# Performance work log

Measured on AMD Instinct MI355X. Metric: run time of the kernel, lower is better.

## Reference

```python
import jax, jax.numpy as jnp
import numpy as np

N_NODES = 50000
N_EDGES = 800000
DIM_IN = 128
DIM_OUT = 64


def setup_inputs() -> dict:
    key = jax.random.key(0)
    k1, k2, k3, k4 = jax.random.split(key, 4)
    x = jax.random.normal(k1, (N_NODES, DIM_IN), dtype=jnp.float32)
    edge_index = jax.random.randint(k2, (2, N_EDGES), 0, N_NODES, dtype=jnp.int64)
    W = jax.random.normal(k3, (DIM_IN, DIM_OUT), dtype=jnp.float32) / np.sqrt(DIM_IN)
    b = jax.random.normal(k4, (DIM_OUT,), dtype=jnp.float32) * 0.01
    return {"x": x, "edge_index": edge_index, "W": W, "b": b}


def reference(x, edge_index, W, b):
    # Faithful PyG GCNConv: add self-loops, symmetric deg normalization,
    # linear transform then normalized scatter-add aggregation, then bias.
    N = x.shape[0]
    h = x @ W  # [N, dim_out] — transform before propagate (PyG order)

    loops = jnp.arange(N, dtype=edge_index.dtype)
    src = jnp.concatenate([edge_index[0], loops])  # [E+N]
    dst = jnp.concatenate([edge_index[1], loops])  # [E+N]

    ones = jnp.ones(src.shape[0], dtype=h.dtype)
    deg = jax.ops.segment_sum(ones, dst, num_segments=N)  # in-degree incl. self-loop
    dinv = jnp.where(deg > 0, jax.lax.rsqrt(deg), 0.0)
    norm = dinv[src] * dinv[dst]  # [E+N]

    msgs = h[src] * norm[:, None]  # gather + scale
    out = jax.ops.segment_sum(msgs, dst, num_segments=N) + b  # scatter-add
    return jax.nn.log_softmax(out, axis=1)
```

## Files before the change

### kernel.cpp

```cpp
#include <hip/hip_runtime.h>
#include <hip/hip_fp16.h>
#include <cstdint>
#include <cstddef>

#define N_NODES 50000
#define N_EDGES 800000
#define DIM_IN  128
#define DIM_OUT 64

#define B2SHIFT 8
#define B2NODES 256
#define NB2     ((N_NODES + B2NODES - 1) / B2NODES)
#define EB      4096
#define SORTB   ((N_EDGES + EB - 1) / EB)
#define NE4     (N_EDGES / 4)
#define CAPB    4864
#define GROWS   512
#define GEMMB   ((N_NODES + GROWS - 1) / GROWS)
#define GPAD    16
#define NEGRP   ((N_NODES + 31) / 32)

typedef _Float16 f16x8 __attribute__((ext_vector_type(8)));
typedef float    f32x4 __attribute__((ext_vector_type(4)));

__global__ __launch_bounds__(256) void k_zero(int* __restrict__ gcnt) {
    const int i = blockIdx.x * 256 + threadIdx.x;
    if (i < NB2 * GPAD) gcnt[i] = 0;
}

__global__ __launch_bounds__(1024) void kFG(const int* __restrict__ ei,
                                            int* __restrict__ gcnt,
                                            unsigned* __restrict__ pairs,
                                            const float* __restrict__ x,
                                            const float* __restrict__ W,
                                            __half* __restrict__ h) {
    const int t = threadIdx.x;
    if (blockIdx.x < SORTB) {
        __shared__ int hcnt[B2NODES];
        __shared__ int excl[B2NODES];
        __shared__ int curb[B2NODES];
        __shared__ int gbase[B2NODES];
        __shared__ int wsum[4];
        __shared__ unsigned lpair[EB];
        const int blk = blockIdx.x;
        const int ecnt = min(EB, N_EDGES - blk * EB);
        if (t < B2NODES) hcnt[t] = 0;
        __syncthreads();
        const int4* src4 = (const int4*)ei;
        const int4* dst4 = (const int4*)(ei + N_EDGES);
        const int g = blk * (EB / 4) + t;
        int4 sv, dv;
        const bool live = (g < NE4);
        if (live) {
            dv = dst4[g];
            sv = src4[g];
            atomicAdd(&hcnt[dv.x >> B2SHIFT], 1);
            atomicAdd(&hcnt[dv.y >> B2SHIFT], 1);
            atomicAdd(&hcnt[dv.z >> B2SHIFT], 1);
            atomicAdd(&hcnt[dv.w >> B2SHIFT], 1);
        }
        __syncthreads();
        if (t < B2NODES) {
            const int lane = t & 63;
            const int v = hcnt[t];
            int xs = v;
#pragma unroll
            for (int off = 1; off < 64; off <<= 1) {
                int y = __shfl_up(xs, off);
                if (lane >= off) xs += y;
            }
            excl[t] = xs;
            if (lane == 63) wsum[t >> 6] = xs;
        }
        __syncthreads();
        if (t == 0) {
            int acc = 0;
#pragma unroll
            for (int w2 = 0; w2 < 4; ++w2) { const int v2 = wsum[w2]; wsum[w2] = acc; acc += v2; }
        }
        __syncthreads();
        if (t < B2NODES) {
            const int v = hcnt[t];
            const int e = excl[t] - v + wsum[t >> 6];
            excl[t] = e;
            curb[t] = e;
            const int base = v ? atomicAdd(&gcnt[t * GPAD], v) : 0;
            gbase[t] = t * CAPB + base - e;
        }
        __syncthreads();
        if (live) {
            int b, p;
            b = dv.x >> B2SHIFT; p = atomicAdd(&curb[b], 1);
            lpair[p] = ((unsigned)sv.x << 16) | (unsigned)dv.x;
            b = dv.y >> B2SHIFT; p = atomicAdd(&curb[b], 1);
            lpair[p] = ((unsigned)sv.y << 16) | (unsigned)dv.y;
            b = dv.z >> B2SHIFT; p = atomicAdd(&curb[b], 1);
            lpair[p] = ((unsigned)sv.z << 16) | (unsigned)dv.z;
            b = dv.w >> B2SHIFT; p = atomicAdd(&curb[b], 1);
            lpair[p] = ((unsigned)sv.w << 16) | (unsigned)dv.w;
        }
        __syncthreads();
        for (int j = t; j < ecnt; j += 1024) {
            const unsigned p = lpair[j];
            const int b = (int)(p & 0xFFFFu) >> B2SHIFT;
            const int dst = gbase[b] + j;
            if (dst < (b + 1) * CAPB) pairs[dst] = p;
        }
    } else {
        const int u = blockIdx.x - SORTB;
        const int w = t >> 6;
        const int l = t & 63;
        const int q = l >> 4;
        const int m16 = l & 15;

        f16x8 bf[4][4];
#pragma unroll
        for (int kc = 0; kc < 4; ++kc)
#pragma unroll
            for (int ct = 0; ct < 4; ++ct) {
                const float* wp = W + (size_t)(kc * 32 + q * 8) * DIM_OUT + ct * 16 + m16;
                f16x8 v;
#pragma unroll
                for (int j = 0; j < 8; ++j) v[j] = (_Float16)wp[(size_t)j * DIM_OUT];
                bf[kc][ct] = v;
            }

        const int base = u * GROWS + w * 32;
#pragma unroll
        for (int rt = 0; rt < 2; ++rt) {
            const int m0 = base + rt * 16;
            int mrow = m0 + m16;
            if (mrow >= N_NODES) mrow = N_NODES - 1;

            f16x8 af[4];
#pragma unroll
            for (int kc = 0; kc < 4; ++kc) {
                const float4* xp = (const float4*)(x + (size_t)mrow * DIM_IN + kc * 32 + q * 8);
                const float4 p0 = xp[0], p1 = xp[1];
                f16x8 a;
                a[0] = (_Float16)p0.x; a[1] = (_Float16)p0.y;
                a[2] = (_Float16)p0.z; a[3] = (_Float16)p0.w;
                a[4] = (_Float16)p1.x; a[5] = (_Float16)p1.y;
                a[6] = (_Float16)p1.z; a[7] = (_Float16)p1.w;
                af[kc] = a;
            }

            f32x4 acc[4];
#pragma unroll
            for (int ct = 0; ct < 4; ++ct) acc[ct] = (f32x4){0.f, 0.f, 0.f, 0.f};
#pragma unroll
            for (int kc = 0; kc < 4; ++kc)
#pragma unroll
                for (int ct = 0; ct < 4; ++ct)
                    acc[ct] = __builtin_amdgcn_mfma_f32_16x16x32_f16(af[kc], bf[kc][ct], acc[ct], 0, 0, 0);

#pragma unroll
            for (int reg = 0; reg < 4; ++reg) {
                const int r = m0 + q * 4 + reg;
                if (r < N_NODES) {
#pragma unroll
                    for (int ct = 0; ct < 4; ++ct)
                        h[(size_t)r * DIM_OUT + ct * 16 + m16] = __float2half(acc[ct][reg]);
                }
            }
        }
    }
}

__global__ __launch_bounds__(512) void kSort(const unsigned* __restrict__ pairs,
                                             const int* __restrict__ gcnt,
                                             unsigned short* __restrict__ csr,
                                             int2* __restrict__ nodeoff2,
                                             __half* __restrict__ h) {
    __shared__ int cnt[B2NODES];
    __shared__ int cur[B2NODES];
    __shared__ float sdinv[B2NODES];
    __shared__ int wsum[4];
    __shared__ unsigned short lcsr[CAPB];
    const int b = blockIdx.x, t = threadIdx.x;
    const int eb = b * CAPB;
    const int count = min(gcnt[b * GPAD], CAPB);
    const int ee = eb + count;

    if (t < B2NODES) cnt[t] = 0;
    __syncthreads();

    {
        int i = eb + t;
        for (; i + 1536 < ee; i += 2048) {
            const unsigned p0 = pairs[i];
            const unsigned p1 = pairs[i + 512];
            const unsigned p2 = pairs[i + 1024];
            const unsigned p3 = pairs[i + 1536];
            atomicAdd(&cnt[p0 & (B2NODES - 1)], 1);
            atomicAdd(&cnt[p1 & (B2NODES - 1)], 1);
            atomicAdd(&cnt[p2 & (B2NODES - 1)], 1);
            atomicAdd(&cnt[p3 & (B2NODES - 1)], 1);
        }
        for (; i < ee; i += 512) atomicAdd(&cnt[pairs[i] & (B2NODES - 1)], 1);
    }
    __syncthreads();

    if (t < B2NODES) {
        const int lane = t & 63;
        const int v = cnt[t];
        int xs = v;
#pragma unroll
        for (int off = 1; off < 64; off <<= 1) {
            int y = __shfl_up(xs, off);
            if (lane >= off) xs += y;
        }
        cur[t] = xs;
        if (lane == 63) wsum[t >> 6] = xs;
    }
    __syncthreads();
    if (t == 0) {
        int acc = 0;
#pragma unroll
        for (int w2 = 0; w2 < 4; ++w2) { const int v2 = wsum[w2]; wsum[w2] = acc; acc += v2; }
    }
    __syncthreads();
    if (t < B2NODES) {
        const int v = cnt[t];
        const int excl = cur[t] - v + wsum[t >> 6];
        sdinv[t] = rsqrtf((float)(v + 1));
        const int n = (b << B2SHIFT) + t;
        if (n < N_NODES) nodeoff2[n] = make_int2(eb + excl, v);
        cur[t] = excl;
    }
    __syncthreads();

    for (int i = eb + t; i < ee; i += 512) {
        const unsigned p = pairs[i];
        const int q = atomicAdd(&cur[p & (B2NODES - 1)], 1);
        lcsr[q] = (unsigned short)(p >> 16);
    }
    __syncthreads();

    {
        const int cw = (count + 1) >> 1;
        const unsigned* l32 = (const unsigned*)lcsr;
        unsigned* c32 = (unsigned*)(csr + eb);
        for (int i2 = t; i2 < cw; i2 += 512) c32[i2] = l32[i2];
    }
    {
        f16x8* h8w = (f16x8*)h;
        for (int idx = t; idx < B2NODES * 8; idx += 512) {
            const int r = idx >> 3;
            const int n = (b << B2SHIFT) + r;
            if (n < N_NODES) {
                const float d = sdinv[r];
                f16x8 v = h8w[(size_t)n * 8 + (idx & 7)];
#pragma unroll
                for (int j = 0; j < 8; ++j) v[j] = (_Float16)((float)v[j] * d);
                h8w[(size_t)n * 8 + (idx & 7)] = v;
            }
        }
    }
}

__global__ __launch_bounds__(256) void kE_agg(const int2* __restrict__ nodeoff2,
                                              const unsigned short* __restrict__ csr,
                                              const __half* __restrict__ h,
                                              const float* __restrict__ bvec,
                                              float* __restrict__ out) {
    const int t = threadIdx.x;
    const int ew = t >> 3, sl = t & 7;
    const int n = blockIdx.x * 32 + ew;
    if (n >= N_NODES) return;
    const f16x8* __restrict__ h8 = (const f16x8*)h;

    const int2 off = nodeoff2[n];
    const int s0 = off.x, s1 = off.x + off.y;

    const f16x8 hv = h8[(size_t)n * 8 + sl];
    float a[8];
#pragma unroll
    for (int j = 0; j < 8; ++j) a[j] = (float)hv[j];

    int i = s0;
    for (; i + 4 <= s1; i += 4) {
        const int c0 = csr[i + 0];
        const int c1 = csr[i + 1];
        const int c2 = csr[i + 2];
        const int c3 = csr[i + 3];
        const f16x8 v0 = h8[(size_t)c0 * 8 + sl];
        const f16x8 v1 = h8[(size_t)c1 * 8 + sl];
        const f16x8 v2 = h8[(size_t)c2 * 8 + sl];
        const f16x8 v3 = h8[(size_t)c3 * 8 + sl];
#pragma unroll
        for (int j = 0; j < 8; ++j)
            a[j] += (float)v0[j] + (float)v1[j] + (float)v2[j] + (float)v3[j];
    }
    for (; i < s1; ++i) {
        const f16x8 v0 = h8[(size_t)csr[i] * 8 + sl];
#pragma unroll
        for (int j = 0; j < 8; ++j) a[j] += (float)v0[j];
    }

    const float4 b0 = *(const float4*)&bvec[8 * sl];
    const float4 b1 = *(const float4*)&bvec[8 * sl + 4];
    const float di = rsqrtf((float)(off.y + 1));
    float v[8];
    v[0] = a[0] * di + b0.x; v[1] = a[1] * di + b0.y;
    v[2] = a[2] * di + b0.z; v[3] = a[3] * di + b0.w;
    v[4] = a[4] * di + b1.x; v[5] = a[5] * di + b1.y;
    v[6] = a[6] * di + b1.z; v[7] = a[7] * di + b1.w;

    float m = v[0];
#pragma unroll
    for (int j = 1; j < 8; ++j) m = fmaxf(m, v[j]);
#pragma unroll
    for (int o = 4; o > 0; o >>= 1) m = fmaxf(m, __shfl_xor(m, o));
    float s = 0.f;
#pragma unroll
    for (int j = 0; j < 8; ++j) s += __expf(v[j] - m);
#pragma unroll
    for (int o = 4; o > 0; o >>= 1) s += __shfl_xor(s, o);
    const float ls = m + __logf(s);

    float4 o0, o1;
    o0.x = v[0] - ls; o0.y = v[1] - ls; o0.z = v[2] - ls; o0.w = v[3] - ls;
    o1.x = v[4] - ls; o1.y = v[5] - ls; o1.z = v[6] - ls; o1.w = v[7] - ls;
    *(float4*)&out[(size_t)n * DIM_OUT + 8 * sl]     = o0;
    *(float4*)&out[(size_t)n * DIM_OUT + 8 * sl + 4] = o1;
}

extern "C" void kernel_launch(void* const* d_in, const int* in_sizes, int n_in,
                              void* d_out, int out_size, void* d_ws, size_t ws_size,
                              hipStream_t stream) {
    const float* x  = (const float*)d_in[0];
    const int*   ei = (const int*)d_in[1];
    const float* W  = (const float*)d_in[2];
    const float* b  = (const float*)d_in[3];
    float* out = (float*)d_out;

    char* ws = (char*)d_ws;
    __half*         h        = (__half*)ws;         ws += (size_t)N_NODES * DIM_OUT * sizeof(__half);
    unsigned*       pairs    = (unsigned*)ws;       ws += (size_t)NB2 * CAPB * sizeof(unsigned);
    unsigned short* csr      = (unsigned short*)ws; ws += (size_t)NB2 * CAPB * sizeof(unsigned short);
    int2*           nodeoff2 = (int2*)ws;           ws += (size_t)N_NODES * sizeof(int2);
    int*            gcnt     = (int*)ws;            ws += (size_t)NB2 * GPAD * sizeof(int);

    k_zero <<<(NB2 * GPAD + 255) / 256, 256, 0, stream>>>(gcnt);
    kFG    <<<SORTB + GEMMB, 1024, 0, stream>>>(ei, gcnt, pairs, x, W, h);
    kSort  <<<NB2, 512, 0, stream>>>(pairs, gcnt, csr, nodeoff2, h);
    kE_agg <<<NEGRP, 256, 0, stream>>>(nodeoff2, csr, h, b, out);
}
```

Before: 122.3 us.

## Replace global atomic bucket counters with per-block histogram and deterministic prefix scatter

Splits the fused histogram+scatter stage into a histogram kernel (fused with the GEMM) that writes per-block bucket counts, and a separate scatter kernel that computes each block's global offsets by summing earlier blocks' histograms. This removes the zeroing kernel and global atomics on bucket counters, and makes pair placement deterministic. The cost is an extra kernel launch, the edge index being read twice, and an O(SORTB) serial prefix loop per bucket thread in kScatter. kSort now reduces the histogram column to get its bucket total. GEMM blocks shrink to 256 threads with 128 rows each.

```diff
diff --git a/kernel.cpp b/kernel.cpp
--- a/kernel.cpp
+++ b/kernel.cpp
@@ -15,80 +15,155 @@
 #define SORTB   ((N_EDGES + EB - 1) / EB)
 #define NE4     (N_EDGES / 4)
 #define CAPB    4864
-#define GROWS   512
+#define GROWS   128
 #define GEMMB   ((N_NODES + GROWS - 1) / GROWS)
-#define GPAD    16
+#define HSTRIDE 256
 #define NEGRP   ((N_NODES + 31) / 32)
 
 typedef _Float16 f16x8 __attribute__((ext_vector_type(8)));
 typedef float    f32x4 __attribute__((ext_vector_type(4)));
 
-__global__ __launch_bounds__(256) void k_zero(int* __restrict__ gcnt) {
-    const int i = blockIdx.x * 256 + threadIdx.x;
-    if (i < NB2 * GPAD) gcnt[i] = 0;
-}
-
-__global__ __launch_bounds__(1024) void kFG(const int* __restrict__ ei,
-                                            int* __restrict__ gcnt,
-                                            unsigned* __restrict__ pairs,
-                                            const float* __restrict__ x,
-                                            const float* __restrict__ W,
-                                            __half* __restrict__ h) {
+__global__ __launch_bounds__(256) void k1_histgemm(const int* __restrict__ ei,
+                                                   int* __restrict__ hist,
+                                                   const float* __restrict__ x,
+                                                   const float* __restrict__ W,
+                                                   __half* __restrict__ h) {
     const int t = threadIdx.x;
     if (blockIdx.x < SORTB) {
         __shared__ int hcnt[B2NODES];
-        __shared__ int excl[B2NODES];
-        __shared__ int curb[B2NODES];
-        __shared__ int gbase[B2NODES];
-        __shared__ int wsum[4];
-        __shared__ unsigned lpair[EB];
         const int blk = blockIdx.x;
-        const int ecnt = min(EB, N_EDGES - blk * EB);
-        if (t < B2NODES) hcnt[t] = 0;
+        hcnt[t] = 0;
         __syncthreads();
+        const int4* dst4 = (const int4*)(ei + N_EDGES);
+        const int g0 = blk * (EB / 4);
+#pragma unroll
+        for (int it = 0; it < EB / 1024; ++it) {
+            const int g = g0 + it * 256 + t;
+            if (g < NE4) {
+                const int4 d = dst4[g];
+                atomicAdd(&hcnt[d.x >> B2SHIFT], 1);
+                atomicAdd(&hcnt[d.y >> B2SHIFT], 1);
+                atomicAdd(&hcnt[d.z >> B2SHIFT], 1);
+                atomicAdd(&hcnt[d.w >> B2SHIFT], 1);
+            }
+        }
+        __syncthreads();
+        hist[blk * HSTRIDE + t] = hcnt[t];
+    } else {
+        const int u = blockIdx.x - SORTB;
+        const int w = t >> 6;
+        const int l = t & 63;
+        const int q = l >> 4;
+        const int m16 = l & 15;
+
+        f16x8 bf[4][4];
+#pragma unroll
+        for (int kc = 0; kc < 4; ++kc)
+#pragma unroll
+            for (int ct = 0; ct < 4; ++ct) {
+                const float* wp = W + (size_t)(kc * 32 + q * 8) * DIM_OUT + ct * 16 + m16;
+                f16x8 v;
+#pragma unroll
+                for (int j = 0; j < 8; ++j) v[j] = (_Float16)wp[(size_t)j * DIM_OUT];
+                bf[kc][ct] = v;
+            }
+
+        const int base = u * GROWS + w * 32;
+#pragma unroll
+        for (int rt = 0; rt < 2; ++rt) {
+            const int m0 = base + rt * 16;
+            int mrow = m0 + m16;
+            if (mrow >= N_NODES) mrow = N_NODES - 1;
+
+            f16x8 af[4];
+#pragma unroll
+            for (int kc = 0; kc < 4; ++kc) {
+                const float4* xp = (const float4*)(x + (size_t)mrow * DIM_IN + kc * 32 + q * 8);
+                const float4 p0 = xp[0], p1 = xp[1];
+                f16x8 a;
+                a[0] = (_Float16)p0.x; a[1] = (_Float16)p0.y;
+                a[2] = (_Float16)p0.z; a[3] = (_Float16)p0.w;
+                a[4] = (_Float16)p1.x; a[5] = (_Float16)p1.y;
+                a[6] = (_Float16)p1.z; a[7] = (_Float16)p1.w;
+                af[kc] = a;
+            }
+
+            f32x4 acc[4];
+#pragma unroll
+            for (int ct = 0; ct < 4; ++ct) acc[ct] = (f32x4){0.f, 0.f, 0.f, 0.f};
+#pragma unroll
+            for (int kc = 0; kc < 4; ++kc)
+#pragma unroll
+                for (int ct = 0; ct < 4; ++ct)
+                    acc[ct] = __builtin_amdgcn_mfma_f32_16x16x32_f16(af[kc], bf[kc][ct], acc[ct], 0, 0, 0);
+
+#pragma unroll
+            for (int reg = 0; reg < 4; ++reg) {
+                const int r = m0 + q * 4 + reg;
+                if (r < N_NODES) {
+#pragma unroll
+                    for (int ct = 0; ct < 4; ++ct)
+                        h[(size_t)r * DIM_OUT + ct * 16 + m16] = __float2half(acc[ct][reg]);
+                }
+            }
+        }
+    }
+}
+
+__global__ __launch_bounds__(512) void kScatter(const int* __restrict__ ei,
+                                                const int* __restrict__ hist,
+                                                unsigned* __restrict__ pairs) {
+    __shared__ int hrow[B2NODES];
+    __shared__ int excl[B2NODES];
+    __shared__ int curb[B2NODES];
+    __shared__ int gbase[B2NODES];
+    __shared__ int wsum[4];
+    __shared__ unsigned lpair[EB];
+    const int blk = blockIdx.x, t = threadIdx.x;
+    const int ecnt = min(EB, N_EDGES - blk * EB);
+
+    if (t < B2NODES) {
+        hrow[t] = hist[blk * HSTRIDE + t];
+        int s = 0;
+        for (int tt = 0; tt < blk; ++tt)
+            s += hist[tt * HSTRIDE + t];
+        gbase[t] = s;
+    }
+    __syncthreads();
+    if (t < B2NODES) {
+        const int lane = t & 63;
+        const int v = hrow[t];
+        int xs = v;
+#pragma unroll
+        for (int off = 1; off < 64; off <<= 1) {
+            int y = __shfl_up(xs, off);
+            if (lane >= off) xs += y;
+        }
+        excl[t] = xs;
+        if (lane == 63) wsum[t >> 6] = xs;
+    }
+    __syncthreads();
+    if (t == 0) {
+        int acc = 0;
+#pragma unroll
+        for (int w2 = 0; w2 < 4; ++w2) { const int v2 = wsum[w2]; wsum[w2] = acc; acc += v2; }
+    }
+    __syncthreads();
+    if (t < B2NODES) {
+        const int e = excl[t] - hrow[t] + wsum[t >> 6];
+        excl[t] = e;
+        curb[t] = e;
+        gbase[t] = t * CAPB + gbase[t] - e;
+    }
+    __syncthreads();
+    {
         const int4* src4 = (const int4*)ei;
         const int4* dst4 = (const int4*)(ei + N_EDGES);
-        const int g = blk * (EB / 4) + t;
-        int4 sv, dv;
-        const bool live = (g < NE4);
-        if (live) {
-            dv = dst4[g];
-            sv = src4[g];
-            atomicAdd(&hcnt[dv.x >> B2SHIFT], 1);
-            atomicAdd(&hcnt[dv.y >> B2SHIFT], 1);
-            atomicAdd(&hcnt[dv.z >> B2SHIFT], 1);
-            atomicAdd(&hcnt[dv.w >> B2SHIFT], 1);
-        }
-        __syncthreads();
-        if (t < B2NODES) {
-            const int lane = t & 63;
-            const int v = hcnt[t];
-            int xs = v;
-#pragma unroll
-            for (int off = 1; off < 64; off <<= 1) {
-                int y = __shfl_up(xs, off);
-                if (lane >= off) xs += y;
-            }
-            excl[t] = xs;
-            if (lane == 63) wsum[t >> 6] = xs;
-        }
-        __syncthreads();
-        if (t == 0) {
-            int acc = 0;
-#pragma unroll
-            for (int w2 = 0; w2 < 4; ++w2) { const int v2 = wsum[w2]; wsum[w2] = acc; acc += v2; }
-        }
-        __syncthreads();
-        if (t < B2NODES) {
-            const int v = hcnt[t];
-            const int e = excl[t] - v + wsum[t >> 6];
-            excl[t] = e;
-            curb[t] = e;
-            const int base = v ? atomicAdd(&gcnt[t * GPAD], v) : 0;
-            gbase[t] = t * CAPB + base - e;
-        }
-        __syncthreads();
-        if (live) {
+        const int gA = blk * (EB / 4) + t;
+        const int gB = gA + 512;
+        const int glim = blk * (EB / 4) + (ecnt >> 2);
+        if (gA < glim && gA < NE4) {
+            const int4 dv = dst4[gA]; const int4 sv = src4[gA];
             int b, p;
             b = dv.x >> B2SHIFT; p = atomicAdd(&curb[b], 1);
             lpair[p] = ((unsigned)sv.x << 16) | (unsigned)dv.x;
@@ -99,76 +174,30 @@
             b = dv.w >> B2SHIFT; p = atomicAdd(&curb[b], 1);
             lpair[p] = ((unsigned)sv.w << 16) | (unsigned)dv.w;
         }
-        __syncthreads();
-        for (int j = t; j < ecnt; j += 1024) {
-            const unsigned p = lpair[j];
-            const int b = (int)(p & 0xFFFFu) >> B2SHIFT;
-            const int dst = gbase[b] + j;
-            if (dst < (b + 1) * CAPB) pairs[dst] = p;
-        }
-    } else {
-        const int u = blockIdx.x - SORTB;
-        const int w = t >> 6;
-        const int l = t & 63;
-        const int q = l >> 4;
-        const int m16 = l & 15;
-
-        f16x8 bf[4][4];
-#pragma unroll
-        for (int kc = 0; kc < 4; ++kc)
-#pragma unroll
-            for (int ct = 0; ct < 4; ++ct) {
-                const float* wp = W + (size_t)(kc * 32 + q * 8) * DIM_OUT + ct * 16 + m16;
-                f16x8 v;
-#pragma unroll
-                for (int j = 0; j < 8; ++j) v[j] = (_Float16)wp[(size_t)j * DIM_OUT];
-                bf[kc][ct] = v;
-            }
-
-        const int base = u * GROWS + w * 32;
-#pragma unroll
-        for (int rt = 0; rt < 2; ++rt) {
-            const int m0 = base + rt * 16;
-            int mrow = m0 + m16;
-            if (mrow >= N_NODES) mrow = N_NODES - 1;
-
-            f16x8 af[4];
-#pragma unroll
-            for (int kc = 0; kc < 4; ++kc) {
-                const float4* xp = (const float4*)(x + (size_t)mrow * DIM_IN + kc * 32 + q * 8);
-                const float4 p0 = xp[0], p1 = xp[1];
-                f16x8 a;
-                a[0] = (_Float16)p0.x; a[1] = (_Float16)p0.y;
-                a[2] = (_Float16)p0.z; a[3] = (_Float16)p0.w;
-                a[4] = (_Float16)p1.x; a[5] = (_Float16)p1.y;
-                a[6] = (_Float16)p1.z; a[7] = (_Float16)p1.w;
-                af[kc] = a;
-            }
-
-            f32x4 acc[4];
-#pragma unroll
-            for (int ct = 0; ct < 4; ++ct) acc[ct] = (f32x4){0.f, 0.f, 0.f, 0.f};
-#pragma unroll
-            for (int kc = 0; kc < 4; ++kc)
-#pragma unroll
-                for (int ct = 0; ct < 4; ++ct)
-                    acc[ct] = __builtin_amdgcn_mfma_f32_16x16x32_f16(af[kc], bf[kc][ct], acc[ct], 0, 0, 0);
-
-#pragma unroll
-            for (int reg = 0; reg < 4; ++reg) {
-                const int r = m0 + q * 4 + reg;
-                if (r < N_NODES) {
-#pragma unroll
-                    for (int ct = 0; ct < 4; ++ct)
-                        h[(size_t)r * DIM_OUT + ct * 16 + m16] = __float2half(acc[ct][reg]);
-                }
-            }
-        }
+        if (gB < glim && gB < NE4) {
+            const int4 dv = dst4[gB]; const int4 sv = src4[gB];
+            int b, p;
+            b = dv.x >> B2SHIFT; p = atomicAdd(&curb[b], 1);
+            lpair[p] = ((unsigned)sv.x << 16) | (unsigned)dv.x;
+            b = dv.y >> B2SHIFT; p = atomicAdd(&curb[b], 1);
+            lpair[p] = ((unsigned)sv.y << 16) | (unsigned)dv.y;
+            b = dv.z >> B2SHIFT; p = atomicAdd(&curb[b], 1);
+            lpair[p] = ((unsigned)sv.z << 16) | (unsigned)dv.z;
+            b = dv.w >> B2SHIFT; p = atomicAdd(&curb[b], 1);
+            lpair[p] = ((unsigned)sv.w << 16) | (unsigned)dv.w;
+        }
+    }
+    __syncthreads();
+    for (int j = t; j < ecnt; j += 512) {
+        const unsigned p = lpair[j];
+        const int b = (int)(p & 0xFFFFu) >> B2SHIFT;
+        const int dst = gbase[b] + j;
+        if (dst < (b + 1) * CAPB) pairs[dst] = p;
     }
 }
 
 __global__ __launch_bounds__(512) void kSort(const unsigned* __restrict__ pairs,
-                                             const int* __restrict__ gcnt,
+                                             const int* __restrict__ hist,
                                              unsigned short* __restrict__ csr,
                                              int2* __restrict__ nodeoff2,
                                              __half* __restrict__ h) {
@@ -176,14 +205,24 @@
     __shared__ int cur[B2NODES];
     __shared__ float sdinv[B2NODES];
     __shared__ int wsum[4];
+    __shared__ int btot;
     __shared__ unsigned short lcsr[CAPB];
     const int b = blockIdx.x, t = threadIdx.x;
     const int eb = b * CAPB;
-    const int count = min(gcnt[b * GPAD], CAPB);
+
+    {
+        int v = 0;
+        for (int tt = t; tt < SORTB; tt += 512) v += hist[tt * HSTRIDE + b];
+#pragma unroll
+        for (int off = 32; off > 0; off >>= 1) v += __shfl_xor(v, off);
+        if ((t & 63) == 0) wsum[t >> 6] = v;
+        __syncthreads();
+        if (t == 0) btot = min(wsum[0] + wsum[1] + wsum[2] + wsum[3], CAPB);
+    }
+    if (t < B2NODES) cnt[t] = 0;
+    __syncthreads();
+    const int count = btot;
     const int ee = eb + count;
-
-    if (t < B2NODES) cnt[t] = 0;
-    __syncthreads();
 
     {
         int i = eb + t;
@@ -340,10 +379,10 @@
     unsigned*       pairs    = (unsigned*)ws;       ws += (size_t)NB2 * CAPB * sizeof(unsigned);
     unsigned short* csr      = (unsigned short*)ws; ws += (size_t)NB2 * CAPB * sizeof(unsigned short);
     int2*           nodeoff2 = (int2*)ws;           ws += (size_t)N_NODES * sizeof(int2);
-    int*            gcnt     = (int*)ws;            ws += (size_t)NB2 * GPAD * sizeof(int);
-
-    k_zero <<<(NB2 * GPAD + 255) / 256, 256, 0, stream>>>(gcnt);
-    kFG    <<<SORTB + GEMMB, 1024, 0, stream>>>(ei, gcnt, pairs, x, W, h);
-    kSort  <<<NB2, 512, 0, stream>>>(pairs, gcnt, csr, nodeoff2, h);
-    kE_agg <<<NEGRP, 256, 0, stream>>>(nodeoff2, csr, h, b, out);
-}
+    int*            hist     = (int*)ws;            ws += (size_t)SORTB * HSTRIDE * sizeof(int);
+
+    k1_histgemm<<<SORTB + GEMMB, 256, 0, stream>>>(ei, hist, x, W, h);
+    kScatter   <<<SORTB, 512, 0, stream>>>(ei, hist, pairs);
+    kSort      <<<NB2, 512, 0, stream>>>(pairs, hist, csr, nodeoff2, h);
+    kE_agg     <<<NEGRP, 256, 0, stream>>>(nodeoff2, csr, h, b, out);
+}
```

Measured after the change: 138.9 us. 1.14x slower.
